# Optimization experiments

Hardware: AMD Instinct MI355X
Metric: run time of the kernel (lower is better)

Reference implementation:

```python
import jax, jax.numpy as jnp
import numpy as np
from jax import lax

K = 3        # KBA kernel size
GC = 4       # channels per group numerator (gc in torch code): g = c // GC
EPS = 1e-6   # LayerNorm2d eps


def conv2d(x, w, b=None, pad=0, groups=1):
    out = lax.conv_general_dilated(x, w, (1, 1), [(pad, pad), (pad, pad)],
                                   dimension_numbers=('NCHW', 'OIHW', 'NCHW'),
                                   feature_group_count=groups)
    return out if b is None else out + b[None, :, None, None]


def layernorm2d(x, w, b):
    mu = jnp.mean(x, axis=1, keepdims=True)
    var = jnp.mean((x - mu) ** 2, axis=1, keepdims=True)
    y = (x - mu) / jnp.sqrt(var + EPS)
    return w[None, :, None, None] * y + b[None, :, None, None]


def kba_fn(x, att, selfb, selfw):
    # x: (B,c,H,W) features; att: (B,nset,H,W) mixing coeffs
    B, c, H, W = x.shape
    nset = att.shape[1]
    g = c // GC; cg = GC; KK = K * K
    a = att.reshape(B, nset, H * W).transpose(0, 2, 1)              # (B,HW,nset)
    bias = a @ selfb[0]                                             # (B,HW,c)
    attk = (a @ selfw[0]).reshape(B, H * W, g, cg, cg * KK)         # per-pixel kernels
    pad = K // 2
    xp = jnp.pad(x, ((0, 0), (0, 0), (pad, pad), (pad, pad)))
    # im2col / unfold, channel-major then kernel position (matches torch unfold)
    patches = jnp.stack([xp[:, :, i:i + H, j:j + W] for i in range(K) for j in range(K)], axis=2)  # (B,c,KK,H,W)
    uf = patches.reshape(B, g, cg * KK, H * W).transpose(0, 3, 1, 2)  # (B,HW,g,cg*KK)
    out = jnp.einsum('bpgij,bpgj->bpgi', attk, uf).reshape(B, H * W, c) + bias
    return out.transpose(0, 2, 1).reshape(B, c, H, W)


def petformer(x, n1w, n1b, n2w, n2b,
              kdw1, kdw2, kc1a, kc1b, kproj,
              c2a_w, c2a_b, c2b_w, c2b_b, c211_w, c211_b,
              kw, kb, attgamma, ga1,
              temp, qkv_w, qkv_dw_w, mproj_w,
              ca1_w, ca1_b, ca2_w, ca2_b):
    B, C, H, W = x.shape
    # channel attention: global avg pool + 1x1 conv
    gap = jnp.mean(x, axis=(2, 3), keepdims=True)
    ca1 = conv2d(gap, ca1_w, ca1_b)
    ca2 = conv2d(gap, ca2_w, ca2_b)

    # ---- KBA branch ----
    xn = layernorm2d(x, n1w, n1b)
    hid = kdw1.shape[0]
    x1 = conv2d(conv2d(xn, kdw1), kdw2, pad=1, groups=hid)          # dwconv path
    interc = c2a_w.shape[0]
    a = conv2d(xn, c2a_w, c2a_b, pad=1, groups=interc)              # grouped 3x3
    a1, a2 = jnp.split(a, 2, axis=1)                                # SimpleGate
    a = conv2d(a1 * a2, c2b_w, c2b_b)                               # 1x1 -> nset
    att = a * attgamma + conv2d(xn, c211_w, c211_b)
    uf = conv2d(conv2d(xn, kc1a), kc1b, pad=1, groups=hid)          # conv1 path
    x2 = kba_fn(uf, att, kb, kw) * ga1 + uf
    kba_out = conv2d(jax.nn.gelu(x1, approximate=False) * x2, kproj)

    # ---- MDTA branch (transposed channel attention) ----
    xm = layernorm2d(x, n2w, n2b)
    qkv = conv2d(conv2d(xm, qkv_w), qkv_dw_w, pad=1, groups=3 * C)
    q, k, v = jnp.split(qkv, 3, axis=1)
    heads = temp.shape[0]
    _h = lambda t: t.reshape(B, heads, C // heads, H * W)
    q, k, v = _h(q), _h(k), _h(v)
    q = q / jnp.maximum(jnp.linalg.norm(q, axis=-1, keepdims=True), 1e-12)
    k = k / jnp.maximum(jnp.linalg.norm(k, axis=-1, keepdims=True), 1e-12)
    attn = jax.nn.softmax(jnp.einsum('bhcp,bhdp->bhcd', q, k) * temp, axis=-1)
    out = jnp.einsum('bhcd,bhdp->bhcp', attn, v).reshape(B, C, H, W)
    mdta_out = conv2d(out, mproj_w)

    return x + kba_out * ca1 + mdta_out * ca2


def setup_inputs() -> dict:
    key = jax.random.key(0)
    ks = iter(jax.random.split(key, 40))
    nrm = lambda shape, s=0.1: (jax.random.normal(next(ks), shape) * s).astype(jnp.float32)
    B, C, H, W = 4, 48, 64, 64
    HID, NSET, HEADS, INTERC = 96, 32, 8, 24
    return {
        'x': jax.random.normal(next(ks), (B, C, H, W), jnp.float32),
        'n1w': jnp.ones((C,), jnp.float32), 'n1b': jnp.zeros((C,), jnp.float32),
        'n2w': jnp.ones((C,), jnp.float32), 'n2b': jnp.zeros((C,), jnp.float32),
        'kdw1': nrm((HID, C, 1, 1)), 'kdw2': nrm((HID, 1, 3, 3)),
        'kc1a': nrm((HID, C, 1, 1)), 'kc1b': nrm((HID, 1, 3, 3)),
        'kproj': nrm((C, HID, 1, 1)),
        'c2a_w': nrm((INTERC, C // INTERC, 3, 3)), 'c2a_b': jnp.zeros((INTERC,), jnp.float32),
        'c2b_w': nrm((NSET, INTERC // 2, 1, 1)), 'c2b_b': jnp.zeros((NSET,), jnp.float32),
        'c211_w': nrm((NSET, C, 1, 1)), 'c211_b': jnp.zeros((NSET,), jnp.float32),
        'kw': nrm((1, NSET, HID * GC * K * K), 0.02), 'kb': nrm((1, NSET, HID), 0.02),
        'attgamma': jnp.full((1, NSET, 1, 1), 0.01, jnp.float32),
        'ga1': jnp.full((1, HID, 1, 1), 0.01, jnp.float32),
        'temp': jnp.ones((HEADS, 1, 1), jnp.float32),
        'qkv_w': nrm((3 * C, C, 1, 1)), 'qkv_dw_w': nrm((3 * C, 1, 3, 3)),
        'mproj_w': nrm((C, C, 1, 1)),
        'ca1_w': nrm((C, C, 1, 1)), 'ca1_b': jnp.zeros((C,), jnp.float32),
        'ca2_w': nrm((C, C, 1, 1)), 'ca2_b': jnp.zeros((C,), jnp.float32),
    }


def reference(x, n1w, n1b, n2w, n2b,
              kdw1, kdw2, kc1a, kc1b, kproj,
              c2a_w, c2a_b, c2b_w, c2b_b, c211_w, c211_b,
              kw, kb, attgamma, ga1,
              temp, qkv_w, qkv_dw_w, mproj_w,
              ca1_w, ca1_b, ca2_w, ca2_b):
    return petformer(x, n1w, n1b, n2w, n2b, kdw1, kdw2, kc1a, kc1b, kproj,
                     c2a_w, c2a_b, c2b_w, c2b_b, c211_w, c211_b,
                     kw, kb, attgamma, ga1, temp, qkv_w, qkv_dw_w, mproj_w,
                     ca1_w, ca1_b, ca2_w, ca2_b)
```

## Files before the change

kernel.cpp:

```cpp
#include <hip/hip_runtime.h>
#include <hip/hip_bf16.h>
#include <cstdint>

typedef unsigned short ushortT;
typedef __attribute__((ext_vector_type(8))) short short8;
typedef __attribute__((ext_vector_type(4))) float f32x4;
typedef __attribute__((ext_vector_type(4))) unsigned short ushort4v;

static constexpr int Bn = 4, Cc = 48, Hh = 64, Wd = 64, HW = 4096;
static constexpr int HID = 96, NSET = 32, INTERC = 24, HEADS = 8, CPH = 6;

static constexpr int FXN   = 0;
static constexpr int FA    = 786432;
static constexpr int FB    = 2359296;
static constexpr int FC    = 3932160;
static constexpr int FD    = 5505024;
static constexpr int FARAW = 7077888;
static constexpr int FATT  = 7471104;
static constexpr int FGAP  = 8781824;
static constexpr int FSP   = 8782400;
static constexpr int FW    = 8790000;
static constexpr int FATTB = 8937200;
static constexpr int FWT   = 9199344;
static constexpr int FXNB  = 9260784;
static constexpr int FXMB  = 9785072;
static constexpr int FHBF  = 10309360;
static constexpr int FWPW  = 11095792;
static constexpr int FWQK  = 11102960;
static constexpr int FWKP  = 11107568;
static constexpr int FWMP  = 11109872;
static constexpr int FQKVR = 11111424;
static constexpr int FQKV  = 13470720;

static constexpr int W_N1W=0, W_N1B=48, W_N2W=96, W_N2B=144;
static constexpr int W_KDW1=192, W_KDW2=4800, W_KC1A=5664, W_KC1B=10272;
static constexpr int W_KPROJ=11136, W_C2AW=15744, W_C2AB=16176;
static constexpr int W_C2BW=16200, W_C2BB=16584, W_C211W=16616, W_C211B=18152;
static constexpr int W_KW=18184, W_KB=128776, W_ATTG=131848, W_GA1=131880;
static constexpr int W_TEMP=131976, W_QKVW=131984, W_QKVDW=138896, W_MPROJ=140192;
static constexpr int W_CA1W=142496, W_CA1B=144800, W_CA2W=144848, W_CA2B=147152;

__device__ __forceinline__ float b2f(ushortT u) {
    union { uint32_t i; float f; } v; v.i = ((uint32_t)u) << 16; return v.f;
}
__device__ __forceinline__ ushortT f2b(float f) {
    union { float f; uint32_t i; } v; v.f = f;
    uint32_t i = v.i;
    uint32_t lsb = (i >> 16) & 1u;
    i += 0x7fffu + lsb;
    return (ushortT)(i >> 16);
}
__device__ __forceinline__ int dtype_bf16(const uint32_t* n1w_raw) {
    return n1w_raw[0] == 0x3F803F80u;
}
__device__ __forceinline__ ushortT raw_bf(const void* p, int idx, int fl) {
    return fl ? ((const ushortT*)p)[idx] : f2b(((const float*)p)[idx]);
}
__device__ __forceinline__ float raw_f(const void* p, int idx, int fl) {
    return fl ? b2f(((const ushortT*)p)[idx]) : ((const float*)p)[idx];
}

struct ConvPack {
    const void* src[27];
    int dstoff[27];
    int n[27];
};
struct RawW {
    const void* kdw1; const void* kc1a; const void* c211w; const void* qkvw;
    const void* kproj; const void* mproj; const void* kw; const void* kb;
    const void* n1w; const void* n1b; const void* n2w; const void* n2b;
};

__global__ void __launch_bounds__(256) k_prep(ConvPack p, RawW rw, float* __restrict__ dst,
                       ushortT* __restrict__ Wt, ushortT* __restrict__ Wpw,
                       ushortT* __restrict__ Wqk, ushortT* __restrict__ Wkp,
                       ushortT* __restrict__ Wmp,
                       const void* __restrict__ x, float* __restrict__ gap,
                       ushortT* __restrict__ xn, ushortT* __restrict__ xnb,
                       ushortT* __restrict__ xmb,
                       const uint32_t* __restrict__ n1w_raw) {
    int fl = dtype_bf16(n1w_raw);
    int y = blockIdx.y;
    if (y < 27) {
        int n = p.n[y];
        for (int i = blockIdx.x * 256 + threadIdx.x; i < n; i += 64 * 256) {
            dst[p.dstoff[y] + i] = raw_f(p.src[y], i, fl);
        }
    } else if (y == 27) {
        for (int u = blockIdx.x * 256 + threadIdx.x; u < 24 * 160 * 32; u += 64 * 256) {
            int n = u & 31;
            int rest = u >> 5;
            int r = rest % 160;
            int gr = rest / 160;
            ushortT out;
            if (r < 144) {
                int j = r >> 2, i = r & 3;
                out = raw_bf(rw.kw, n * 3456 + gr * 144 + i * 36 + j, fl);
            } else if (r < 148) {
                out = raw_bf(rw.kb, n * HID + gr * 4 + (r - 144), fl);
            } else out = 0;
            Wt[u] = out;
        }
    } else if (y == 28) {
        for (int u = blockIdx.x * 256 + threadIdx.x; u < 224 * 64; u += 64 * 256) {
            int co = u >> 6, c = u & 63;
            ushortT v = 0;
            if (c < 48) {
                if (co < 96)       v = raw_bf(rw.kdw1,  co * 48 + c, fl);
                else if (co < 192) v = raw_bf(rw.kc1a,  (co - 96) * 48 + c, fl);
                else               v = raw_bf(rw.c211w, (co - 192) * 48 + c, fl);
            }
            Wpw[u] = v;
        }
    } else if (y == 29) {
        for (int u = blockIdx.x * 256 + threadIdx.x; u < 144 * 64; u += 64 * 256) {
            int co = u >> 6, c = u & 63;
            Wqk[u] = (c < 48) ? raw_bf(rw.qkvw, co * 48 + c, fl) : (ushortT)0;
        }
    } else if (y == 30) {
        for (int u = blockIdx.x * 256 + threadIdx.x; u < 48 * 96; u += 64 * 256) {
            int co = u / 96, c = u % 96;
            Wkp[u] = raw_bf(rw.kproj, co * 96 + c, fl);
        }
    } else if (y == 31) {
        for (int u = blockIdx.x * 256 + threadIdx.x; u < 48 * 64; u += 64 * 256) {
            int co = u >> 6, c = u & 63;
            Wmp[u] = (c < 48) ? raw_bf(rw.mproj, co * 48 + c, fl) : (ushortT)0;
        }
    } else if (y == 32) {
        __shared__ float red[4];
        for (int bc = blockIdx.x; bc < Bn * Cc; bc += 64) {
            float s = 0.f;
            if (fl) {
                const ushortT* xb = (const ushortT*)x + bc * HW;
                for (int i = threadIdx.x; i < HW; i += 256) s += b2f(xb[i]);
            } else {
                const float* xb = (const float*)x + bc * HW;
                for (int i = threadIdx.x; i < HW; i += 256) s += xb[i];
            }
            #pragma unroll
            for (int o = 32; o > 0; o >>= 1) s += __shfl_down(s, o);
            int lane = threadIdx.x & 63, wv = threadIdx.x >> 6;
            if (lane == 0) red[wv] = s;
            __syncthreads();
            if (threadIdx.x == 0)
                gap[bc] = (red[0] + red[1] + red[2] + red[3]) * (1.f / HW);
            __syncthreads();
        }
    } else {
        int slice = y - 33;
        int tid = threadIdx.x;
        int pp = slice * 4096 + blockIdx.x * 64 + (tid >> 2);
        int part = tid & 3;
        int b = pp >> 12, hw = pp & 4095;
        const ushortT* xbh = (const ushortT*)x + (size_t)b * Cc * HW + hw;
        const float*  xbf = (const float*)x + (size_t)b * Cc * HW + hw;
        float v[12];
        float s = 0.f, ss = 0.f;
        #pragma unroll
        for (int j = 0; j < 12; j++) {
            int c = part * 12 + j;
            float t = fl ? b2f(xbh[c * HW]) : xbf[c * HW];
            v[j] = t; s += t; ss += t * t;
        }
        s  += __shfl_xor(s, 1);  s  += __shfl_xor(s, 2);
        ss += __shfl_xor(ss, 1); ss += __shfl_xor(ss, 2);
        float mu = s * (1.f / Cc);
        float var = ss * (1.f / Cc) - mu * mu;
        float r = rsqrtf(var + 1e-6f);
        uint32_t wn[6], wm[6];
        #pragma unroll
        for (int j2 = 0; j2 < 6; j2++) {
            int c0 = part * 12 + j2 * 2;
            float y0 = (v[j2 * 2] - mu) * r, y1 = (v[j2 * 2 + 1] - mu) * r;
            float n0 = raw_f(rw.n1w, c0, fl) * y0 + raw_f(rw.n1b, c0, fl);
            float n1 = raw_f(rw.n1w, c0 + 1, fl) * y1 + raw_f(rw.n1b, c0 + 1, fl);
            float m0 = raw_f(rw.n2w, c0, fl) * y0 + raw_f(rw.n2b, c0, fl);
            float m1 = raw_f(rw.n2w, c0 + 1, fl) * y1 + raw_f(rw.n2b, c0 + 1, fl);
            ushortT hn0 = f2b(n0), hn1 = f2b(n1);
            xn[(size_t)(b * Cc + c0) * HW + hw] = hn0;
            xn[(size_t)(b * Cc + c0 + 1) * HW + hw] = hn1;
            wn[j2] = (uint32_t)hn0 | ((uint32_t)hn1 << 16);
            wm[j2] = (uint32_t)f2b(m0) | ((uint32_t)f2b(m1) << 16);
        }
        uint32_t* dn = (uint32_t*)(xnb + (size_t)pp * 64 + part * 12);
        uint32_t* dm = (uint32_t*)(xmb + (size_t)pp * 64 + part * 12);
        #pragma unroll
        for (int j2 = 0; j2 < 6; j2++) { dn[j2] = wn[j2]; dm[j2] = wm[j2]; }
        if (part == 3) {
            uint4 zz; zz.x = 0; zz.y = 0; zz.z = 0; zz.w = 0;
            *(uint4*)(xnb + (size_t)pp * 64 + 48) = zz;
            *(uint4*)(xmb + (size_t)pp * 64 + 48) = zz;
        }
    }
}

__global__ void __launch_bounds__(256) k_pw1m(const ushortT* __restrict__ xnb, const ushortT* __restrict__ xmb,
                       const ushortT* __restrict__ Wpw, const ushortT* __restrict__ Wqk,
                       const float* __restrict__ wts, ushortT* __restrict__ t1,
                       ushortT* __restrict__ t2, ushortT* __restrict__ attn_t,
                       ushortT* __restrict__ qkvr) {
    int wave = threadIdx.x >> 6, lane = threadIdx.x & 63;
    int m = lane & 15, q = lane >> 4;
    int p = blockIdx.x * 64 + wave * 16 + m;
    int b = p >> 12, hw = p & 4095;
    if (blockIdx.y == 0) {
        short8 B0 = *(const short8*)(xnb + (size_t)p * 64 + q * 8);
        short8 B1 = *(const short8*)(xnb + (size_t)p * 64 + 32 + q * 8);
        #pragma unroll
        for (int t = 0; t < 14; t++) {
            short8 A0 = *(const short8*)(Wpw + (16 * t + m) * 64 + q * 8);
            short8 A1 = *(const short8*)(Wpw + (16 * t + m) * 64 + 32 + q * 8);
            f32x4 z = {0.f, 0.f, 0.f, 0.f};
            f32x4 D = __builtin_amdgcn_mfma_f32_16x16x32_bf16(A0, B0, z, 0, 0, 0);
            D = __builtin_amdgcn_mfma_f32_16x16x32_bf16(A1, B1, D, 0, 0, 0);
            #pragma unroll
            for (int g = 0; g < 4; g++) {
                int co = 16 * t + 4 * q + g;
                if (t < 6) t1[(size_t)(b * HID + co) * HW + hw] = f2b(D[g]);
                else if (t < 12) t2[(size_t)(b * HID + (co - 96)) * HW + hw] = f2b(D[g]);
                else {
                    int n = co - 192;
                    attn_t[(size_t)p * 32 + n] = f2b(D[g] + wts[W_C211B + n]);
                }
            }
        }
    } else {
        short8 C0 = *(const short8*)(xmb + (size_t)p * 64 + q * 8);
        short8 C1 = *(const short8*)(xmb + (size_t)p * 64 + 32 + q * 8);
        #pragma unroll
        for (int t = 0; t < 9; t++) {
            short8 A0 = *(const short8*)(Wqk + (16 * t + m) * 64 + q * 8);
            short8 A1 = *(const short8*)(Wqk + (16 * t + m) * 64 + 32 + q * 8);
            f32x4 z = {0.f, 0.f, 0.f, 0.f};
            f32x4 D = __builtin_amdgcn_mfma_f32_16x16x32_bf16(A0, C0, z, 0, 0, 0);
            D = __builtin_amdgcn_mfma_f32_16x16x32_bf16(A1, C1, D, 0, 0, 0);
            #pragma unroll
            for (int g = 0; g < 4; g++) {
                int co = 16 * t + 4 * q + g;
                qkvr[(size_t)(b * 144 + co) * HW + hw] = f2b(D[g]);
            }
        }
    }
}

__device__ __forceinline__ void row4_bf(const ushortT* row, int w0,
                                        float& lf, float& m0, float& m1,
                                        float& m2, float& m3, float& rt) {
    ushort4v mm = *(const ushort4v*)row;
    m0 = b2f(mm[0]); m1 = b2f(mm[1]); m2 = b2f(mm[2]); m3 = b2f(mm[3]);
    lf = (w0 > 0)  ? b2f(row[-1]) : 0.f;
    rt = (w0 < 60) ? b2f(row[4])  : 0.f;
}

__global__ void __launch_bounds__(256) k_dw(const ushortT* __restrict__ t1, const ushortT* __restrict__ t2,
                     const ushortT* __restrict__ xn, const ushortT* __restrict__ qkvr,
                     const float* __restrict__ wts,
                     ushortT* __restrict__ x1g, ushortT* __restrict__ uf,
                     ushortT* __restrict__ araw, ushortT* __restrict__ qkv) {
    int y = blockIdx.y;
    int pbase = blockIdx.x * 1024 + threadIdx.x * 4;
    int b = pbase >> 12, hw = pbase & 4095, h = hw >> 6, w0 = hw & 63;

    if (y < 192) {
        int c = (y < 96) ? y : y - 96;
        const ushortT* base = (y < 96) ? t1 : t2;
        const float* wk = wts + ((y < 96) ? W_KDW2 : W_KC1B) + c * 9;
        const ushortT* plane = base + (size_t)(b * HID + c) * HW;

        float a0 = 0.f, a1 = 0.f, a2 = 0.f, a3 = 0.f;
        #pragma unroll
        for (int ki = 0; ki < 3; ki++) {
            int hh = h + ki - 1;
            if ((unsigned)hh < 64u) {
                const ushortT* row = plane + hh * 64 + w0;
                float lf, m0, m1, m2, m3, rt;
                row4_bf(row, w0, lf, m0, m1, m2, m3, rt);
                float k0 = wk[ki * 3], k1 = wk[ki * 3 + 1], k2 = wk[ki * 3 + 2];
                a0 += k0 * lf + k1 * m0 + k2 * m1;
                a1 += k0 * m0 + k1 * m1 + k2 * m2;
                a2 += k0 * m1 + k1 * m2 + k2 * m3;
                a3 += k0 * m2 + k1 * m3 + k2 * rt;
            }
        }
        size_t idx = (size_t)(b * HID + c) * HW + hw;
        ushort4v o;
        if (y < 96) {
            o[0] = f2b(0.5f * a0 * (1.f + erff(a0 * 0.70710678118654752f)));
            o[1] = f2b(0.5f * a1 * (1.f + erff(a1 * 0.70710678118654752f)));
            o[2] = f2b(0.5f * a2 * (1.f + erff(a2 * 0.70710678118654752f)));
            o[3] = f2b(0.5f * a3 * (1.f + erff(a3 * 0.70710678118654752f)));
            *(ushort4v*)(x1g + idx) = o;
        } else {
            o[0] = f2b(a0); o[1] = f2b(a1); o[2] = f2b(a2); o[3] = f2b(a3);
            *(ushort4v*)(uf + idx) = o;
        }
    } else if (y < 216) {
        int o = y - 192;
        float bias = wts[W_C2AB + o];
        float a0 = bias, a1 = bias, a2 = bias, a3 = bias;
        #pragma unroll
        for (int ic = 0; ic < 2; ic++) {
            const ushortT* plane = xn + (size_t)(b * Cc + 2 * o + ic) * HW;
            const float* wk = wts + W_C2AW + (o * 2 + ic) * 9;
            #pragma unroll
            for (int ki = 0; ki < 3; ki++) {
                int hh = h + ki - 1;
                if ((unsigned)hh < 64u) {
                    const ushortT* row = plane + hh * 64 + w0;
                    float lf, m0, m1, m2, m3, rt;
                    row4_bf(row, w0, lf, m0, m1, m2, m3, rt);
                    float k0 = wk[ki * 3], k1 = wk[ki * 3 + 1], k2 = wk[ki * 3 + 2];
                    a0 += k0 * lf + k1 * m0 + k2 * m1;
                    a1 += k0 * m0 + k1 * m1 + k2 * m2;
                    a2 += k0 * m1 + k1 * m2 + k2 * m3;
                    a3 += k0 * m2 + k1 * m3 + k2 * rt;
                }
            }
        }
        ushort4v out;
        out[0] = f2b(a0); out[1] = f2b(a1); out[2] = f2b(a2); out[3] = f2b(a3);
        *(ushort4v*)(araw + (size_t)(b * INTERC + o) * HW + hw) = out;
    } else {
        int ch = y - 216;
        const float* wk = wts + W_QKVDW + ch * 9;
        const ushortT* plane = qkvr + (size_t)(b * 144 + ch) * HW;

        float a0 = 0.f, a1 = 0.f, a2 = 0.f, a3 = 0.f;
        #pragma unroll
        for (int ki = 0; ki < 3; ki++) {
            int hh = h + ki - 1;
            if ((unsigned)hh < 64u) {
                const ushortT* row = plane + hh * 64 + w0;
                float lf, m0, m1, m2, m3, rt;
                row4_bf(row, w0, lf, m0, m1, m2, m3, rt);
                float k0 = wk[ki * 3], k1 = wk[ki * 3 + 1], k2 = wk[ki * 3 + 2];
                a0 += k0 * lf + k1 * m0 + k2 * m1;
                a1 += k0 * m0 + k1 * m1 + k2 * m2;
                a2 += k0 * m1 + k1 * m2 + k2 * m3;
                a3 += k0 * m2 + k1 * m3 + k2 * rt;
            }
        }
        ushort4v o;
        o[0] = f2b(a0); o[1] = f2b(a1); o[2] = f2b(a2); o[3] = f2b(a3);
        *(ushort4v*)(qkv + (size_t)(b * 144 + ch) * HW + hw) = o;
    }
}

__global__ void __launch_bounds__(256) k_attsm(const ushortT* __restrict__ araw, const ushortT* __restrict__ attn_t,
                       const ushortT* __restrict__ qkv, const float* __restrict__ wts,
                       ushortT* __restrict__ att_bf, float* __restrict__ Sp) {
    if (blockIdx.x < 64) {
        int p = blockIdx.x * 256 + threadIdx.x;
        int b = p >> 12, hw = p & 4095;
        const ushortT* ab = araw + (size_t)b * INTERC * HW + hw;
        float sg[12];
        #pragma unroll
        for (int i = 0; i < 12; i++) sg[i] = b2f(ab[i * HW]) * b2f(ab[(12 + i) * HW]);
        const ushortT* ct = attn_t + (size_t)p * 32;
        uint32_t packed[16];
        #pragma unroll
        for (int nq = 0; nq < 16; nq++) {
            float v2[2];
            #pragma unroll
            for (int u = 0; u < 2; u++) {
                int n = nq * 2 + u;
                float a = wts[W_C2BB + n];
                #pragma unroll
                for (int c = 0; c < 12; c++) a += wts[W_C2BW + n * 12 + c] * sg[c];
                v2[u] = wts[W_ATTG + n] * a + b2f(ct[n]);
            }
            packed[nq] = (uint32_t)f2b(v2[0]) | ((uint32_t)f2b(v2[1]) << 16);
        }
        uint4* dst = (uint4*)(att_bf + (size_t)p * 32);
        #pragma unroll
        for (int qd = 0; qd < 4; qd++) {
            uint4 v; v.x = packed[qd*4]; v.y = packed[qd*4+1]; v.z = packed[qd*4+2]; v.w = packed[qd*4+3];
            dst[qd] = v;
        }
    } else {
        int sub = blockIdx.x - 64;
        int bh = sub & 31, chunk = sub >> 5;
        int b = bh / HEADS, hd = bh % HEADS;
        const ushortT* qb = qkv + (size_t)(b * 144 + hd * CPH) * HW;
        const ushortT* kb = qkv + (size_t)(b * 144 + 48 + hd * CPH) * HW;
        float acc[48];
        #pragma unroll
        for (int t = 0; t < 48; t++) acc[t] = 0.f;
        #pragma unroll
        for (int i = 0; i < 4; i++) {
            int px = chunk * 1024 + i * 256 + threadIdx.x;
            float qv[CPH], kv[CPH];
            #pragma unroll
            for (int c = 0; c < CPH; c++) { qv[c] = b2f(qb[c * HW + px]); kv[c] = b2f(kb[c * HW + px]); }
            #pragma unroll
            for (int c = 0; c < CPH; c++) {
                #pragma unroll
                for (int d = 0; d < CPH; d++) acc[c * CPH + d] += qv[c] * kv[d];
                acc[36 + c] += qv[c] * qv[c];
                acc[42 + c] += kv[c] * kv[c];
            }
        }
        __shared__ float red[48 * 4];
        int lane = threadIdx.x & 63, wv = threadIdx.x >> 6;
        #pragma unroll
        for (int t = 0; t < 48; t++) {
            float v = acc[t];
            #pragma unroll
            for (int o = 32; o > 0; o >>= 1) v += __shfl_down(v, o);
            if (lane == 0) red[t * 4 + wv] = v;
        }
        __syncthreads();
        if (threadIdx.x < 48)
            Sp[(bh * 4 + chunk) * 48 + threadIdx.x] =
                red[threadIdx.x * 4] + red[threadIdx.x * 4 + 1] +
                red[threadIdx.x * 4 + 2] + red[threadIdx.x * 4 + 3];
    }
}

__global__ void __launch_bounds__(256) k_kba(const ushortT* __restrict__ att_bf, const ushortT* __restrict__ uf,
                     const ushortT* __restrict__ x1g, const ushortT* __restrict__ Wt,
                     const float* __restrict__ wts, ushortT* __restrict__ h_bf) {
    int wave = threadIdx.x >> 6, lane = threadIdx.x & 63;
    int m = lane & 15, q = lane >> 4;
    int gr = blockIdx.y;

    short8 A[10];
    const ushortT* wtg = Wt + gr * 160 * 32;
    #pragma unroll
    for (int t = 0; t < 10; t++)
        A[t] = *(const short8*)(wtg + (16 * t + m) * 32 + q * 8);

    for (int tile = 0; tile < 4; tile++) {
        int p = blockIdx.x * 256 + wave * 64 + tile * 16 + m;
        int b = p >> 12, hw = p & 4095, h = hw >> 6, w = hw & 63;

        short8 Bf = *(const short8*)(att_bf + (size_t)p * 32 + q * 8);

        f32x4 D[10];
        #pragma unroll
        for (int t = 0; t < 10; t++) {
            f32x4 z = {0.f, 0.f, 0.f, 0.f};
            D[t] = __builtin_amdgcn_mfma_f32_16x16x32_bf16(A[t], Bf, z, 0, 0, 0);
        }

        float s0 = 0.f, s1 = 0.f, s2 = 0.f, s3 = 0.f;
        #pragma unroll
        for (int t = 0; t < 9; t++) {
            int j = 4 * t + q;
            int ci = j / 9;
            int kk = j - 9 * ci;
            int ki = kk / 3, kj = kk - 3 * ki;
            int hh = h + ki - 1, ww = w + kj - 1;
            float tap = 0.f;
            if ((unsigned)hh < 64u && (unsigned)ww < 64u)
                tap = b2f(uf[(size_t)(b * HID + gr * 4 + ci) * HW + hh * 64 + ww]);
            s0 += D[t][0] * tap;
            s1 += D[t][1] * tap;
            s2 += D[t][2] * tap;
            s3 += D[t][3] * tap;
        }
        s0 += D[9][0]; s1 += D[9][1]; s2 += D[9][2]; s3 += D[9][3];

        s0 += __shfl_xor(s0, 16); s0 += __shfl_xor(s0, 32);
        s1 += __shfl_xor(s1, 16); s1 += __shfl_xor(s1, 32);
        s2 += __shfl_xor(s2, 16); s2 += __shfl_xor(s2, 32);
        s3 += __shfl_xor(s3, 16); s3 += __shfl_xor(s3, 32);

        float sel = (q == 0) ? s0 : ((q == 1) ? s1 : ((q == 2) ? s2 : s3));
        int ch = gr * 4 + q;
        size_t idx = (size_t)(b * HID + ch) * HW + hw;
        float x2 = sel * wts[W_GA1 + ch] + b2f(uf[idx]);
        float hv = b2f(x1g[idx]) * x2;
        h_bf[(size_t)p * 96 + ch] = f2b(hv);
    }
}

__global__ void __launch_bounds__(256) k_finalm(const void* __restrict__ x, const uint32_t* __restrict__ n1w_raw,
                        const ushortT* __restrict__ h_bf, const ushortT* __restrict__ Wkp,
                        const ushortT* __restrict__ Wmp, const ushortT* __restrict__ qkv,
                        const float* __restrict__ Sp, const float* __restrict__ gap,
                        const float* __restrict__ wts, void* __restrict__ out) {
    int fl = dtype_bf16(n1w_raw);
    int wave = threadIdx.x >> 6, lane = threadIdx.x & 63;
    int m = lane & 15, q = lane >> 4;
    int p = blockIdx.x * 64 + wave * 16 + m;
    int hw = p & 4095;
    int wl = wave * 16 + m;
    int bblk = (blockIdx.x * 64) >> 12;
    int hw0 = (blockIdx.x * 64) & 4095;

    __shared__ float sm[384];
    __shared__ float S_l[288];
    __shared__ float caL[96];
    __shared__ ushortT vS[48 * 68];

    for (int i2 = threadIdx.x; i2 < 48 * 64; i2 += 256) {
        int ch = i2 >> 6, w2 = i2 & 63;
        vS[ch * 68 + w2] = qkv[(size_t)(bblk * 144 + 96 + ch) * HW + hw0 + w2];
    }
    for (int i = threadIdx.x; i < 384; i += 256) {
        int hd = i / 48, k = i % 48;
        int bh = bblk * HEADS + hd;
        sm[i] = Sp[(bh * 4 + 0) * 48 + k] + Sp[(bh * 4 + 1) * 48 + k]
              + Sp[(bh * 4 + 2) * 48 + k] + Sp[(bh * 4 + 3) * 48 + k];
    }
    __syncthreads();
    if (threadIdx.x < 48) {
        int hd = threadIdx.x / 6, c = threadIdx.x % 6;
        const float* base = sm + hd * 48;
        float rqv = 1.f / fmaxf(sqrtf(base[36 + c]), 1e-12f);
        float tmp = wts[W_TEMP + hd];
        float row[CPH];
        #pragma unroll
        for (int d = 0; d < CPH; d++) {
            float rkv = 1.f / fmaxf(sqrtf(base[42 + d]), 1e-12f);
            row[d] = base[c * CPH + d] * rqv * rkv * tmp;
        }
        float mx = row[0];
        #pragma unroll
        for (int d = 1; d < CPH; d++) mx = fmaxf(mx, row[d]);
        float sum = 0.f;
        #pragma unroll
        for (int d = 0; d < CPH; d++) { row[d] = expf(row[d] - mx); sum += row[d]; }
        float inv = 1.f / sum;
        #pragma unroll
        for (int d = 0; d < CPH; d++) S_l[hd * 36 + c * CPH + d] = row[d] * inv;
    }
    if (threadIdx.x >= 64 && threadIdx.x < 160) {
        int i = threadIdx.x - 64;
        int which = i / 48, co = i % 48;
        const float* g = gap + bblk * Cc;
        float sacc = wts[(which ? W_CA2B : W_CA1B) + co];
        #pragma unroll
        for (int c = 0; c < Cc; c++)
            sacc += wts[(which ? W_CA2W : W_CA1W) + co * Cc + c] * g[c];
        caL[i] = sacc;
    }
    __syncthreads();

    short8 H0 = *(const short8*)(h_bf + (size_t)p * 96 + q * 8);
    short8 H1 = *(const short8*)(h_bf + (size_t)p * 96 + 32 + q * 8);
    short8 H2 = *(const short8*)(h_bf + (size_t)p * 96 + 64 + q * 8);
    f32x4 Dk[3];
    #pragma unroll
    for (int t = 0; t < 3; t++) {
        short8 A0 = *(const short8*)(Wkp + (16 * t + m) * 96 + q * 8);
        short8 A1 = *(const short8*)(Wkp + (16 * t + m) * 96 + 32 + q * 8);
        short8 A2 = *(const short8*)(Wkp + (16 * t + m) * 96 + 64 + q * 8);
        f32x4 z = {0.f, 0.f, 0.f, 0.f};
        f32x4 D = __builtin_amdgcn_mfma_f32_16x16x32_bf16(A0, H0, z, 0, 0, 0);
        D = __builtin_amdgcn_mfma_f32_16x16x32_bf16(A1, H1, D, 0, 0, 0);
        Dk[t] = __builtin_amdgcn_mfma_f32_16x16x32_bf16(A2, H2, D, 0, 0, 0);
    }

    short8 Bm0, Bm1;
    #pragma unroll
    for (int jj = 0; jj < 8; jj++) {
        int c0 = q * 8 + jj;
        int hd0 = c0 / 6, cc0 = c0 - 6 * hd0;
        float a = 0.f;
        #pragma unroll
        for (int d = 0; d < CPH; d++)
            a += S_l[hd0 * 36 + cc0 * 6 + d] * b2f(vS[(hd0 * 6 + d) * 68 + wl]);
        Bm0[jj] = (short)f2b(a);
        int c1 = 32 + q * 8 + jj;
        float bv = 0.f;
        if (c1 < 48) {
            int hd1 = c1 / 6, cc1 = c1 - 6 * hd1;
            #pragma unroll
            for (int d = 0; d < CPH; d++)
                bv += S_l[hd1 * 36 + cc1 * 6 + d] * b2f(vS[(hd1 * 6 + d) * 68 + wl]);
        }
        Bm1[jj] = (short)f2b(bv);
    }

    #pragma unroll
    for (int t = 0; t < 3; t++) {
        short8 A0 = *(const short8*)(Wmp + (16 * t + m) * 64 + q * 8);
        short8 A1 = *(const short8*)(Wmp + (16 * t + m) * 64 + 32 + q * 8);
        f32x4 z = {0.f, 0.f, 0.f, 0.f};
        f32x4 D = __builtin_amdgcn_mfma_f32_16x16x32_bf16(A0, Bm0, z, 0, 0, 0);
        D = __builtin_amdgcn_mfma_f32_16x16x32_bf16(A1, Bm1, D, 0, 0, 0);
        #pragma unroll
        for (int g = 0; g < 4; g++) {
            int co = 16 * t + 4 * q + g;
            int idx = (bblk * Cc + co) * HW + hw;
            float xv = fl ? b2f(((const ushortT*)x)[idx]) : ((const float*)x)[idx];
            float res = xv + Dk[t][g] * caL[co] + D[g] * caL[48 + co];
            if (fl) ((ushortT*)out)[idx] = f2b(res);
            else    ((float*)out)[idx] = res;
        }
    }
}

extern "C" void kernel_launch(void* const* d_in, const int* in_sizes, int n_in,
                              void* d_out, int out_size, void* d_ws, size_t ws_size,
                              hipStream_t stream) {
    float* ws_f = (float*)d_ws;

    ushortT* xn    = (ushortT*)(ws_f + FXN);
    ushortT* bufA  = (ushortT*)(ws_f + FA);
    ushortT* bufB  = (ushortT*)(ws_f + FB);
    ushortT* x1g   = (ushortT*)(ws_f + FC);
    ushortT* uf    = (ushortT*)(ws_f + FD);
    ushortT* araw  = (ushortT*)(ws_f + FARAW);
    ushortT* attn_t= (ushortT*)(ws_f + FATT);
    float* gap   = ws_f + FGAP;
    float* Sp    = ws_f + FSP;
    float* wts   = ws_f + FW;
    ushortT* att_bf  = (ushortT*)(ws_f + FATTB);
    ushortT* Wt      = (ushortT*)(ws_f + FWT);
    ushortT* xnb     = (ushortT*)(ws_f + FXNB);
    ushortT* xmb     = (ushortT*)(ws_f + FXMB);
    ushortT* h_bf    = (ushortT*)(ws_f + FHBF);
    ushortT* Wpw     = (ushortT*)(ws_f + FWPW);
    ushortT* Wqk     = (ushortT*)(ws_f + FWQK);
    ushortT* Wkp     = (ushortT*)(ws_f + FWKP);
    ushortT* Wmp     = (ushortT*)(ws_f + FWMP);
    ushortT* qkvr    = (ushortT*)(ws_f + FQKVR);
    ushortT* qkv     = (ushortT*)(ws_f + FQKV);

    const uint32_t* n1w_raw = (const uint32_t*)d_in[1];

    static const int wsizes[27] = {48,48,48,48,4608,864,4608,864,4608,432,24,384,32,
                                   1536,32,110592,3072,32,96,8,6912,1296,2304,2304,48,2304,48};
    static const int woffs[27] = {W_N1W,W_N1B,W_N2W,W_N2B,W_KDW1,W_KDW2,W_KC1A,W_KC1B,
                                  W_KPROJ,W_C2AW,W_C2AB,W_C2BW,W_C2BB,W_C211W,W_C211B,
                                  W_KW,W_KB,W_ATTG,W_GA1,W_TEMP,W_QKVW,W_QKVDW,W_MPROJ,
                                  W_CA1W,W_CA1B,W_CA2W,W_CA2B};
    ConvPack cp;
    for (int i = 0; i < 27; i++) {
        cp.src[i] = d_in[i + 1];
        cp.dstoff[i] = woffs[i];
        cp.n[i] = wsizes[i];
    }
    RawW rw;
    rw.kdw1 = d_in[5]; rw.kc1a = d_in[7]; rw.c211w = d_in[14]; rw.qkvw = d_in[21];
    rw.kproj = d_in[9]; rw.mproj = d_in[23]; rw.kw = d_in[16]; rw.kb = d_in[17];
    rw.n1w = d_in[1]; rw.n1b = d_in[2]; rw.n2w = d_in[3]; rw.n2b = d_in[4];

    k_prep<<<dim3(64, 37), 256, 0, stream>>>(cp, rw, wts, Wt, Wpw, Wqk, Wkp, Wmp,
                                             d_in[0], gap, xn, xnb, xmb, n1w_raw);
    k_pw1m<<<dim3(256, 2), 256, 0, stream>>>(xnb, xmb, Wpw, Wqk, wts, bufA, bufB, attn_t, qkvr);
    k_dw<<<dim3(16, 360), 256, 0, stream>>>(bufA, bufB, xn, qkvr, wts, x1g, uf, araw, qkv);
    k_attsm<<<dim3(192), 256, 0, stream>>>(araw, attn_t, qkv, wts, att_bf, Sp);
    k_kba<<<dim3(64, 24), 256, 0, stream>>>(att_bf, uf, x1g, Wt, wts, h_bf);
    k_finalm<<<dim3(256), 256, 0, stream>>>(d_in[0], n1w_raw, h_bf, Wkp, Wmp,
                                            qkv, Sp, gap, wts, d_out);
}
```

Baseline: 205.8 us.

## Fuse attention conv and softmax prep into dw kernel, fold Gram reduction into KBA

Removes the separate k_attsm launch. The grouped 3x3 conv producing the 24 intermediate attention channels is now computed per pixel inside k_dw and immediately consumed to build att_bf, so the araw buffer is no longer written and re-read. The q/k Gram-matrix partial reduction moves into an extra grid row of k_kba, with 2 chunks per head instead of 4. This saves a launch and an intermediate round trip. In exchange, the fused branch does uncoalesced scalar loads and keeps 24 accumulators per thread, and the reduction blocks do twice the work each.

```diff
diff --git a/kernel.cpp b/kernel.cpp
--- a/kernel.cpp
+++ b/kernel.cpp
@@ -15,7 +15,6 @@
 static constexpr int FB    = 2359296;
 static constexpr int FC    = 3932160;
 static constexpr int FD    = 5505024;
-static constexpr int FARAW = 7077888;
 static constexpr int FATT  = 7471104;
 static constexpr int FGAP  = 8781824;
 static constexpr int FSP   = 8782400;
@@ -255,14 +254,14 @@
 
 __global__ void __launch_bounds__(256) k_dw(const ushortT* __restrict__ t1, const ushortT* __restrict__ t2,
                      const ushortT* __restrict__ xn, const ushortT* __restrict__ qkvr,
-                     const float* __restrict__ wts,
+                     const ushortT* __restrict__ attn_t, const float* __restrict__ wts,
                      ushortT* __restrict__ x1g, ushortT* __restrict__ uf,
-                     ushortT* __restrict__ araw, ushortT* __restrict__ qkv) {
+                     ushortT* __restrict__ qkv, ushortT* __restrict__ att_bf) {
     int y = blockIdx.y;
-    int pbase = blockIdx.x * 1024 + threadIdx.x * 4;
-    int b = pbase >> 12, hw = pbase & 4095, h = hw >> 6, w0 = hw & 63;
 
     if (y < 192) {
+        int pbase = blockIdx.x * 1024 + threadIdx.x * 4;
+        int b = pbase >> 12, hw = pbase & 4095, h = hw >> 6, w0 = hw & 63;
         int c = (y < 96) ? y : y - 96;
         const ushortT* base = (y < 96) ? t1 : t2;
         const float* wk = wts + ((y < 96) ? W_KDW2 : W_KC1B) + c * 9;
@@ -295,34 +294,10 @@
             o[0] = f2b(a0); o[1] = f2b(a1); o[2] = f2b(a2); o[3] = f2b(a3);
             *(ushort4v*)(uf + idx) = o;
         }
-    } else if (y < 216) {
-        int o = y - 192;
-        float bias = wts[W_C2AB + o];
-        float a0 = bias, a1 = bias, a2 = bias, a3 = bias;
-        #pragma unroll
-        for (int ic = 0; ic < 2; ic++) {
-            const ushortT* plane = xn + (size_t)(b * Cc + 2 * o + ic) * HW;
-            const float* wk = wts + W_C2AW + (o * 2 + ic) * 9;
-            #pragma unroll
-            for (int ki = 0; ki < 3; ki++) {
-                int hh = h + ki - 1;
-                if ((unsigned)hh < 64u) {
-                    const ushortT* row = plane + hh * 64 + w0;
-                    float lf, m0, m1, m2, m3, rt;
-                    row4_bf(row, w0, lf, m0, m1, m2, m3, rt);
-                    float k0 = wk[ki * 3], k1 = wk[ki * 3 + 1], k2 = wk[ki * 3 + 2];
-                    a0 += k0 * lf + k1 * m0 + k2 * m1;
-                    a1 += k0 * m0 + k1 * m1 + k2 * m2;
-                    a2 += k0 * m1 + k1 * m2 + k2 * m3;
-                    a3 += k0 * m2 + k1 * m3 + k2 * rt;
-                }
-            }
-        }
-        ushort4v out;
-        out[0] = f2b(a0); out[1] = f2b(a1); out[2] = f2b(a2); out[3] = f2b(a3);
-        *(ushort4v*)(araw + (size_t)(b * INTERC + o) * HW + hw) = out;
-    } else {
-        int ch = y - 216;
+    } else if (y < 336) {
+        int pbase = blockIdx.x * 1024 + threadIdx.x * 4;
+        int b = pbase >> 12, hw = pbase & 4095, h = hw >> 6, w0 = hw & 63;
+        int ch = y - 192;
         const float* wk = wts + W_QKVDW + ch * 9;
         const ushortT* plane = qkvr + (size_t)(b * 144 + ch) * HW;
 
@@ -344,19 +319,35 @@
         ushort4v o;
         o[0] = f2b(a0); o[1] = f2b(a1); o[2] = f2b(a2); o[3] = f2b(a3);
         *(ushort4v*)(qkv + (size_t)(b * 144 + ch) * HW + hw) = o;
-    }
-}
-
-__global__ void __launch_bounds__(256) k_attsm(const ushortT* __restrict__ araw, const ushortT* __restrict__ attn_t,
-                       const ushortT* __restrict__ qkv, const float* __restrict__ wts,
-                       ushortT* __restrict__ att_bf, float* __restrict__ Sp) {
-    if (blockIdx.x < 64) {
-        int p = blockIdx.x * 256 + threadIdx.x;
-        int b = p >> 12, hw = p & 4095;
-        const ushortT* ab = araw + (size_t)b * INTERC * HW + hw;
+    } else {
+        int p = (y - 336) * 4096 + blockIdx.x * 256 + threadIdx.x;
+        int b = p >> 12, hw = p & 4095, h = hw >> 6, w0 = hw & 63;
+
+        float av[24];
+        #pragma unroll
+        for (int o = 0; o < 24; o++) {
+            float acc = wts[W_C2AB + o];
+            #pragma unroll
+            for (int ic = 0; ic < 2; ic++) {
+                const ushortT* plane = xn + (size_t)(b * Cc + 2 * o + ic) * HW;
+                const float* wk = wts + W_C2AW + (o * 2 + ic) * 9;
+                #pragma unroll
+                for (int ki = 0; ki < 3; ki++) {
+                    int hh = h + ki - 1;
+                    if ((unsigned)hh < 64u) {
+                        const ushortT* row = plane + hh * 64;
+                        float t0 = (w0 > 0)  ? b2f(row[w0 - 1]) : 0.f;
+                        float t1 = b2f(row[w0]);
+                        float t2 = (w0 < 63) ? b2f(row[w0 + 1]) : 0.f;
+                        acc += wk[ki * 3] * t0 + wk[ki * 3 + 1] * t1 + wk[ki * 3 + 2] * t2;
+                    }
+                }
+            }
+            av[o] = acc;
+        }
         float sg[12];
         #pragma unroll
-        for (int i = 0; i < 12; i++) sg[i] = b2f(ab[i * HW]) * b2f(ab[(12 + i) * HW]);
+        for (int i = 0; i < 12; i++) sg[i] = av[i] * av[12 + i];
         const ushortT* ct = attn_t + (size_t)p * 32;
         uint32_t packed[16];
         #pragma unroll
@@ -378,9 +369,17 @@
             uint4 v; v.x = packed[qd*4]; v.y = packed[qd*4+1]; v.z = packed[qd*4+2]; v.w = packed[qd*4+3];
             dst[qd] = v;
         }
-    } else {
-        int sub = blockIdx.x - 64;
-        int bh = sub & 31, chunk = sub >> 5;
+    }
+}
+
+__global__ void __launch_bounds__(256) k_kba(const ushortT* __restrict__ att_bf, const ushortT* __restrict__ uf,
+                     const ushortT* __restrict__ x1g, const ushortT* __restrict__ Wt,
+                     const ushortT* __restrict__ qkv, const float* __restrict__ wts,
+                     ushortT* __restrict__ h_bf, float* __restrict__ Sp) {
+    __shared__ float red[48 * 4];
+    if (blockIdx.y == 24) {
+        int sub = blockIdx.x;
+        int bh = sub >> 1, chunk = sub & 1;
         int b = bh / HEADS, hd = bh % HEADS;
         const ushortT* qb = qkv + (size_t)(b * 144 + hd * CPH) * HW;
         const ushortT* kb = qkv + (size_t)(b * 144 + 48 + hd * CPH) * HW;
@@ -388,8 +387,8 @@
         #pragma unroll
         for (int t = 0; t < 48; t++) acc[t] = 0.f;
         #pragma unroll
-        for (int i = 0; i < 4; i++) {
-            int px = chunk * 1024 + i * 256 + threadIdx.x;
+        for (int i = 0; i < 8; i++) {
+            int px = chunk * 2048 + i * 256 + threadIdx.x;
             float qv[CPH], kv[CPH];
             #pragma unroll
             for (int c = 0; c < CPH; c++) { qv[c] = b2f(qb[c * HW + px]); kv[c] = b2f(kb[c * HW + px]); }
@@ -401,7 +400,6 @@
                 acc[42 + c] += kv[c] * kv[c];
             }
         }
-        __shared__ float red[48 * 4];
         int lane = threadIdx.x & 63, wv = threadIdx.x >> 6;
         #pragma unroll
         for (int t = 0; t < 48; t++) {
@@ -412,15 +410,12 @@
         }
         __syncthreads();
         if (threadIdx.x < 48)
-            Sp[(bh * 4 + chunk) * 48 + threadIdx.x] =
+            Sp[(bh * 2 + chunk) * 48 + threadIdx.x] =
                 red[threadIdx.x * 4] + red[threadIdx.x * 4 + 1] +
                 red[threadIdx.x * 4 + 2] + red[threadIdx.x * 4 + 3];
-    }
-}
-
-__global__ void __launch_bounds__(256) k_kba(const ushortT* __restrict__ att_bf, const ushortT* __restrict__ uf,
-                     const ushortT* __restrict__ x1g, const ushortT* __restrict__ Wt,
-                     const float* __restrict__ wts, ushortT* __restrict__ h_bf) {
+        return;
+    }
+
     int wave = threadIdx.x >> 6, lane = threadIdx.x & 63;
     int m = lane & 15, q = lane >> 4;
     int gr = blockIdx.y;
@@ -502,8 +497,7 @@
     for (int i = threadIdx.x; i < 384; i += 256) {
         int hd = i / 48, k = i % 48;
         int bh = bblk * HEADS + hd;
-        sm[i] = Sp[(bh * 4 + 0) * 48 + k] + Sp[(bh * 4 + 1) * 48 + k]
-              + Sp[(bh * 4 + 2) * 48 + k] + Sp[(bh * 4 + 3) * 48 + k];
+        sm[i] = Sp[(bh * 2 + 0) * 48 + k] + Sp[(bh * 2 + 1) * 48 + k];
     }
     __syncthreads();
     if (threadIdx.x < 48) {
@@ -604,7 +598,6 @@
     ushortT* bufB  = (ushortT*)(ws_f + FB);
     ushortT* x1g   = (ushortT*)(ws_f + FC);
     ushortT* uf    = (ushortT*)(ws_f + FD);
-    ushortT* araw  = (ushortT*)(ws_f + FARAW);
     ushortT* attn_t= (ushortT*)(ws_f + FATT);
     float* gap   = ws_f + FGAP;
     float* Sp    = ws_f + FSP;
@@ -643,9 +636,8 @@
     k_prep<<<dim3(64, 37), 256, 0, stream>>>(cp, rw, wts, Wt, Wpw, Wqk, Wkp, Wmp,
                                              d_in[0], gap, xn, xnb, xmb, n1w_raw);
     k_pw1m<<<dim3(256, 2), 256, 0, stream>>>(xnb, xmb, Wpw, Wqk, wts, bufA, bufB, attn_t, qkvr);
-    k_dw<<<dim3(16, 360), 256, 0, stream>>>(bufA, bufB, xn, qkvr, wts, x1g, uf, araw, qkv);
-    k_attsm<<<dim3(192), 256, 0, stream>>>(araw, attn_t, qkv, wts, att_bf, Sp);
-    k_kba<<<dim3(64, 24), 256, 0, stream>>>(att_bf, uf, x1g, Wt, wts, h_bf);
+    k_dw<<<dim3(16, 340), 256, 0, stream>>>(bufA, bufB, xn, qkvr, attn_t, wts, x1g, uf, qkv, att_bf);
+    k_kba<<<dim3(64, 25), 256, 0, stream>>>(att_bf, uf, x1g, Wt, qkv, wts, h_bf, Sp);
     k_finalm<<<dim3(256), 256, 0, stream>>>(d_in[0], n1w_raw, h_bf, Wkp, Wmp,
                                             qkv, Sp, gap, wts, d_out);
 }
```

Result: slower. 257.1 us (+24.9%).
